# Kernel optimization log

Measured on AMD Instinct MI355X. Metric: run time of the kernel, lower is better.

## Reference

```python
import jax, jax.numpy as jnp
import numpy as np

NUM_CLASSES = 80
IOU_EPS = 1e-5


def _corners(b):
    # NormalizeBoxes with default shape=ones((2,)) divides by 1 -> plain corner transform
    cx, cy, w, h = b[..., 0], b[..., 1], b[..., 2], b[..., 3]
    return cy - h / 2, cx - w / 2, cy + h / 2, cx + w / 2  # y1, x1, y2, x2


def _pairwise_iou(gt, pr):
    # gt: [B,G,4], pr: [P,4] -> [B,G,P]
    ga = gt[..., 2] * gt[..., 3]                      # [B,G]
    pa = pr[:, 2] * pr[:, 3]                          # [P]
    gy1, gx1, gy2, gx2 = _corners(gt)                 # [B,G]
    py1, px1, py2, px2 = _corners(pr)                 # [P]
    ih = jnp.maximum(0.0, jnp.minimum(gy2[..., None], py2) - jnp.maximum(gy1[..., None], py1))
    iw = jnp.maximum(0.0, jnp.minimum(gx2[..., None], px2) - jnp.maximum(gx1[..., None], px1))
    inter = iw * ih
    union = ga[..., None] + pa - inter
    return inter / (union + IOU_EPS)


def _assign_boxes(gt_boxes, pr_boxes):
    B, G, _ = gt_boxes.shape
    P = pr_boxes.shape[1]
    gt_labels = gt_boxes[..., -2]                     # [B,G]
    gt_conf = gt_boxes[..., -1]                       # [B,G]
    pr = pr_boxes[0].astype(jnp.float32)              # priors shared across batch: [P,4]

    iou = _pairwise_iou(gt_boxes[..., :4].astype(jnp.float32), pr)  # [B,G,P]
    valid = (gt_boxes[..., 0] != -1.0).astype(iou.dtype)
    iou = iou * valid[..., None]

    # matches: all pairs with iou>=0.5, plus the argmax prior per valid (conf>0) GT.
    thresh = iou >= 0.5                                             # [B,G,P]
    best_p = jnp.argmax(iou, axis=-1)                               # [B,G]
    best = (jnp.arange(P)[None, None, :] == best_p[..., None]) & (gt_conf > 0.0)[..., None]

    # thresh matches then best matches -> best overrides thresh; within each
    g_ids = jnp.arange(G)[None, :, None]
    g_thresh = jnp.max(jnp.where(thresh, g_ids, -1), axis=1)        # [B,P]
    g_best = jnp.max(jnp.where(best, g_ids, -1), axis=1)            # [B,P]
    win_g = jnp.where(g_best >= 0, g_best, g_thresh)                # [B,P]
    matched = win_g >= 0

    labels = jnp.take_along_axis(gt_labels, jnp.maximum(win_g, 0), axis=1)  # [B,P]
    cls_id = jnp.where(matched, labels.astype(jnp.int32), NUM_CLASSES)
    onehot = jax.nn.one_hot(cls_id, NUM_CLASSES + 1, dtype=jnp.float32)     # [B,P,C+1]
    assign_mask = onehot[..., -1]                                           # 1 = background
    ignore = jnp.any((iou < 0.5) & (iou >= 0.4), axis=1)                    # [B,P]
    assign_mask = jnp.where(ignore, -1.0, assign_mask)

    # loc targets: tf.scatter_nd SUMS duplicate indices, so each (b,p) target is the
    # sum of encodings over all its matches (thresh + best, duplicates counted twice).
    w = thresh.astype(jnp.float32) + best.astype(jnp.float32)       # [B,G,P]
    gb = gt_boxes[..., :4].astype(jnp.float32)
    safe_log = lambda v: jnp.where(v > 0, jnp.log(jnp.maximum(v, 1e-20)), 0.0)
    W = jnp.sum(w, axis=1)                                          # [B,P] match counts
    S_cx = jnp.einsum('bgp,bg->bp', w, gb[..., 0])
    S_cy = jnp.einsum('bgp,bg->bp', w, gb[..., 1])
    S_lw = jnp.einsum('bgp,bg->bp', w, safe_log(gb[..., 2]))
    S_lh = jnp.einsum('bgp,bg->bp', w, safe_log(gb[..., 3]))
    p_cx, p_cy, p_w, p_h = pr[:, 0], pr[:, 1], pr[:, 2], pr[:, 3]   # [P]
    hat_cx = (S_cx - W * p_cx) / p_w
    hat_cy = (S_cy - W * p_cy) / p_h
    hat_w = S_lw - W * jnp.log(p_w)
    hat_h = S_lh - W * jnp.log(p_h)
    loc_true = jnp.stack([hat_cx, hat_cy, hat_w, hat_h], axis=2)    # [B,P,4]

    cls_true = onehot[..., :NUM_CLASSES]
    return cls_true, loc_true, assign_mask[..., None]


def setup_inputs() -> dict:
    key = jax.random.key(0)
    ks = jax.random.split(key, 8)
    B, G, P = 8, 64, 32768
    NUM_VALID = 48
    g_cx = jax.random.uniform(ks[0], (B, G), minval=0.05, maxval=0.95)
    g_cy = jax.random.uniform(ks[1], (B, G), minval=0.05, maxval=0.95)
    g_w = jax.random.uniform(ks[2], (B, G), minval=0.02, maxval=0.30)
    g_h = jax.random.uniform(ks[3], (B, G), minval=0.02, maxval=0.30)
    labels = jax.random.randint(ks[4], (B, G), 0, NUM_CLASSES).astype(jnp.float32)
    conf = jnp.ones((B, G), dtype=jnp.float32)
    gt = jnp.stack([g_cx, g_cy, g_w, g_h, labels, conf], axis=-1)
    valid = (jnp.arange(G) < NUM_VALID)[None, :, None]
    gt_boxes = jnp.where(valid, gt, -1.0)  # pad trailing GTs with -1 (conf -1 <= 0)
    p_cx = jax.random.uniform(ks[5], (P,), minval=0.0, maxval=1.0)
    p_cy = jax.random.uniform(ks[6], (P,), minval=0.0, maxval=1.0)
    pwh = jax.random.uniform(ks[7], (P, 2), minval=0.02, maxval=0.30)
    pr = jnp.concatenate([p_cx[:, None], p_cy[:, None], pwh], axis=1)
    pr_boxes = jnp.broadcast_to(pr[None], (B, P, 4))
    return {"gt_boxes": gt_boxes, "pr_boxes": pr_boxes}


def reference(gt_boxes, pr_boxes):
    return _assign_boxes(gt_boxes, pr_boxes)
```

## Files before the change

### kernel.cpp

```cpp
#include <hip/hip_runtime.h>
#include <cmath>

#define NBATCH 8
#define NGT    64
#define NPR    32768
#define NC     80

__global__ __launch_bounds__(256) void k_bestp(const float* __restrict__ gt,
                                               const float* __restrict__ pr,
                                               int* __restrict__ bestp) {
#pragma clang fp contract(off)
    const int bg  = blockIdx.x;
    const int tid = threadIdx.x;
    const float* g6 = gt + (size_t)bg * 6;
    const float gcx = g6[0], gcy = g6[1], gw = g6[2], gh = g6[3];
    const bool  valid = (gcx != -1.0f);
    const float gy1 = gcy - gh * 0.5f;
    const float gx1 = gcx - gw * 0.5f;
    const float gy2 = gcy + gh * 0.5f;
    const float gx2 = gcx + gw * 0.5f;
    const float ga  = gw * gh;

    float best = -1.0f;
    int   bidx = 0;
    for (int p = tid; p < NPR; p += 256) {
        float4 pv = ((const float4*)pr)[p];
        float py1 = pv.y - pv.w * 0.5f;
        float px1 = pv.x - pv.z * 0.5f;
        float py2 = pv.y + pv.w * 0.5f;
        float px2 = pv.x + pv.z * 0.5f;
        float pa  = pv.z * pv.w;
        float ih  = fmaxf(0.0f, fminf(gy2, py2) - fmaxf(gy1, py1));
        float iw  = fmaxf(0.0f, fminf(gx2, px2) - fmaxf(gx1, px1));
        float inter = iw * ih;
        float uni   = ga + pa - inter;
        float iou   = inter / (uni + 1e-5f);
        iou = valid ? iou : 0.0f;
        if (iou > best) { best = iou; bidx = p; }
    }

    __shared__ float rv[256];
    __shared__ int   ri[256];
    rv[tid] = best; ri[tid] = bidx;
    __syncthreads();
    for (int s = 128; s > 0; s >>= 1) {
        if (tid < s) {
            float v2 = rv[tid + s]; int i2 = ri[tid + s];
            if (v2 > rv[tid] || (v2 == rv[tid] && i2 < ri[tid])) {
                rv[tid] = v2; ri[tid] = i2;
            }
        }
        __syncthreads();
    }
    if (tid == 0) bestp[bg] = ri[0];
}

__global__ __launch_bounds__(256) void k_assign(const float* __restrict__ gt,
                                                const float* __restrict__ pr,
                                                const int* __restrict__ bestp,
                                                float* __restrict__ out_cls,
                                                float* __restrict__ out_loc,
                                                float* __restrict__ out_msk) {
#pragma clang fp contract(off)
    const int b   = blockIdx.y;
    const int tid = threadIdx.x;
    const int p   = blockIdx.x * 256 + tid;

    __shared__ float s_cx[NGT], s_cy[NGT], s_y1[NGT], s_x1[NGT], s_y2[NGT], s_x2[NGT];
    __shared__ float s_ga[NGT], s_lw[NGT], s_lh[NGT], s_lab[NGT], s_conf[NGT];
    __shared__ int   s_bp[NGT], s_val[NGT];
    __shared__ int   s_cls[256];

    if (tid < NGT) {
        const float* g6 = gt + ((size_t)b * NGT + tid) * 6;
        float cx = g6[0], cy = g6[1], w = g6[2], h = g6[3];
        s_cx[tid] = cx; s_cy[tid] = cy;
        s_y1[tid] = cy - h * 0.5f;
        s_x1[tid] = cx - w * 0.5f;
        s_y2[tid] = cy + h * 0.5f;
        s_x2[tid] = cx + w * 0.5f;
        s_ga[tid] = w * h;
        s_lw[tid] = (w > 0.0f) ? logf(fmaxf(w, 1e-20f)) : 0.0f;
        s_lh[tid] = (h > 0.0f) ? logf(fmaxf(h, 1e-20f)) : 0.0f;
        s_lab[tid]  = g6[4];
        s_conf[tid] = g6[5];
        s_val[tid]  = (cx != -1.0f) ? 1 : 0;
        s_bp[tid]   = bestp[b * NGT + tid];
    }
    __syncthreads();

    float4 pv = ((const float4*)pr)[p];
    const float px = pv.x, py = pv.y, pw = pv.z, ph = pv.w;
    const float py1 = py - ph * 0.5f;
    const float px1 = px - pw * 0.5f;
    const float py2 = py + ph * 0.5f;
    const float px2 = px + pw * 0.5f;
    const float pa  = pw * ph;

    int  g_th = -1, g_bs = -1;
    bool ignore = false;
    float W = 0.0f, Scx = 0.0f, Scy = 0.0f, Slw = 0.0f, Slh = 0.0f;

    for (int g = 0; g < NGT; ++g) {
        float ih = fmaxf(0.0f, fminf(s_y2[g], py2) - fmaxf(s_y1[g], py1));
        float iw = fmaxf(0.0f, fminf(s_x2[g], px2) - fmaxf(s_x1[g], px1));
        float inter = iw * ih;
        float uni   = s_ga[g] + pa - inter;
        float iou   = inter / (uni + 1e-5f);
        iou = s_val[g] ? iou : 0.0f;
        bool th = (iou >= 0.5f);
        bool bs = (s_bp[g] == p) && (s_conf[g] > 0.0f);
        if (th) g_th = g;
        if (bs) g_bs = g;
        ignore = ignore || (iou < 0.5f && iou >= 0.4f);
        float wg = (float)th + (float)bs;
        W   += wg;
        Scx += wg * s_cx[g];
        Scy += wg * s_cy[g];
        Slw += wg * s_lw[g];
        Slh += wg * s_lh[g];
    }

    const int  win     = (g_bs >= 0) ? g_bs : g_th;
    const bool matched = (win >= 0);
    const int  cls     = matched ? (int)s_lab[win] : NC;
    float msk = matched ? 0.0f : 1.0f;
    if (ignore) msk = -1.0f;

    const float hcx = (Scx - W * px) / pw;
    const float hcy = (Scy - W * py) / ph;
    const float hw  = Slw - W * logf(pw);
    const float hh  = Slh - W * logf(ph);

    const size_t bp_i = (size_t)b * NPR + p;
    ((float4*)out_loc)[bp_i] = make_float4(hcx, hcy, hw, hh);
    out_msk[bp_i] = msk;

    s_cls[tid] = cls;
    __syncthreads();
    const size_t base4 = ((size_t)b * NPR + (size_t)blockIdx.x * 256) * NC / 4;
    float4* oc4 = (float4*)out_cls;
    #pragma unroll
    for (int k = 0; k < (256 * NC / 4) / 256; ++k) {
        int idx = tid + k * 256;
        int e0  = idx * 4;
        int pl  = e0 / NC;
        int c0  = e0 - pl * NC;
        int cl  = s_cls[pl];
        float4 v;
        v.x = (c0     == cl) ? 1.0f : 0.0f;
        v.y = (c0 + 1 == cl) ? 1.0f : 0.0f;
        v.z = (c0 + 2 == cl) ? 1.0f : 0.0f;
        v.w = (c0 + 3 == cl) ? 1.0f : 0.0f;
        oc4[base4 + idx] = v;
    }
}

extern "C" void kernel_launch(void* const* d_in, const int* in_sizes, int n_in,
                              void* d_out, int out_size, void* d_ws, size_t ws_size,
                              hipStream_t stream) {
    const float* gt = (const float*)d_in[0];
    const float* pr = (const float*)d_in[1];
    int* bestp = (int*)d_ws;

    float* out_cls = (float*)d_out;
    float* out_loc = out_cls + (size_t)NBATCH * NPR * NC;
    float* out_msk = out_loc + (size_t)NBATCH * NPR * 4;

    k_bestp<<<NBATCH * NGT, 256, 0, stream>>>(gt, pr, bestp);
    dim3 g2(NPR / 256, NBATCH);
    k_assign<<<g2, 256, 0, stream>>>(gt, pr, bestp, out_cls, out_loc, out_msk);
}
```

Measured before the change: 154.1 us.

## Split best-prior argmax into chunked multi-GT blocks with wave-shuffle reduction

The best-prior search now gives each block 8 ground-truth boxes and one of 16 prior chunks. Each prior load is reused across 8 GTs held in registers, and the reduction uses wavefront shuffles instead of a shared-memory tree. Per-chunk partial results go to workspace, and the assign kernel's prologue merges them. The goal is to cut redundant prior reads and sync-heavy reductions, and to use more blocks in parallel. In exchange it adds register pressure and a small extra merge step.

```diff
diff --git a/kernel.cpp b/kernel.cpp
--- a/kernel.cpp
+++ b/kernel.cpp
@@ -6,58 +6,104 @@
 #define NPR    32768
 #define NC     80
 
-__global__ __launch_bounds__(256) void k_bestp(const float* __restrict__ gt,
-                                               const float* __restrict__ pr,
-                                               int* __restrict__ bestp) {
+#define CHUNKS 16
+#define CHUNK  (NPR / CHUNKS)
+#define GTPB   8
+
+__global__ __launch_bounds__(256) void k_bestp_part(const float* __restrict__ gt,
+                                                    const float* __restrict__ pr,
+                                                    float* __restrict__ pval,
+                                                    int* __restrict__ pidx) {
 #pragma clang fp contract(off)
-    const int bg  = blockIdx.x;
-    const int tid = threadIdx.x;
-    const float* g6 = gt + (size_t)bg * 6;
-    const float gcx = g6[0], gcy = g6[1], gw = g6[2], gh = g6[3];
-    const bool  valid = (gcx != -1.0f);
-    const float gy1 = gcy - gh * 0.5f;
-    const float gx1 = gcx - gw * 0.5f;
-    const float gy2 = gcy + gh * 0.5f;
-    const float gx2 = gcx + gw * 0.5f;
-    const float ga  = gw * gh;
-
-    float best = -1.0f;
-    int   bidx = 0;
-    for (int p = tid; p < NPR; p += 256) {
+    const int chunk = blockIdx.x;
+    const int gg    = blockIdx.y;
+    const int tid   = threadIdx.x;
+
+    __shared__ float sy1[GTPB], sx1[GTPB], sy2[GTPB], sx2[GTPB], sga[GTPB];
+    __shared__ int   sv[GTPB];
+    if (tid < GTPB) {
+        const float* g6 = gt + ((size_t)gg * GTPB + tid) * 6;
+        float cx = g6[0], cy = g6[1], w = g6[2], h = g6[3];
+        sy1[tid] = cy - h * 0.5f;
+        sx1[tid] = cx - w * 0.5f;
+        sy2[tid] = cy + h * 0.5f;
+        sx2[tid] = cx + w * 0.5f;
+        sga[tid] = w * h;
+        sv[tid]  = (cx != -1.0f) ? 1 : 0;
+    }
+    __syncthreads();
+
+    float gy1[GTPB], gx1[GTPB], gy2[GTPB], gx2[GTPB], ga[GTPB];
+    int   gv[GTPB];
+    #pragma unroll
+    for (int j = 0; j < GTPB; ++j) {
+        gy1[j] = sy1[j]; gx1[j] = sx1[j]; gy2[j] = sy2[j]; gx2[j] = sx2[j];
+        ga[j] = sga[j]; gv[j] = sv[j];
+    }
+
+    float best[GTPB]; int bi[GTPB];
+    #pragma unroll
+    for (int j = 0; j < GTPB; ++j) { best[j] = -1.0f; bi[j] = 0; }
+
+    const int base = chunk * CHUNK;
+    #pragma unroll 4
+    for (int k = 0; k < CHUNK / 256; ++k) {
+        int p = base + k * 256 + tid;
         float4 pv = ((const float4*)pr)[p];
         float py1 = pv.y - pv.w * 0.5f;
         float px1 = pv.x - pv.z * 0.5f;
         float py2 = pv.y + pv.w * 0.5f;
         float px2 = pv.x + pv.z * 0.5f;
         float pa  = pv.z * pv.w;
-        float ih  = fmaxf(0.0f, fminf(gy2, py2) - fmaxf(gy1, py1));
-        float iw  = fmaxf(0.0f, fminf(gx2, px2) - fmaxf(gx1, px1));
-        float inter = iw * ih;
-        float uni   = ga + pa - inter;
-        float iou   = inter / (uni + 1e-5f);
-        iou = valid ? iou : 0.0f;
-        if (iou > best) { best = iou; bidx = p; }
-    }
-
-    __shared__ float rv[256];
-    __shared__ int   ri[256];
-    rv[tid] = best; ri[tid] = bidx;
-    __syncthreads();
-    for (int s = 128; s > 0; s >>= 1) {
-        if (tid < s) {
-            float v2 = rv[tid + s]; int i2 = ri[tid + s];
-            if (v2 > rv[tid] || (v2 == rv[tid] && i2 < ri[tid])) {
-                rv[tid] = v2; ri[tid] = i2;
+        #pragma unroll
+        for (int j = 0; j < GTPB; ++j) {
+            float ih = fmaxf(0.0f, fminf(gy2[j], py2) - fmaxf(gy1[j], py1));
+            float iw = fmaxf(0.0f, fminf(gx2[j], px2) - fmaxf(gx1[j], px1));
+            float inter = iw * ih;
+            float uni   = ga[j] + pa - inter;
+            float iou   = inter / (uni + 1e-5f);
+            iou = gv[j] ? iou : 0.0f;
+            if (iou > best[j]) { best[j] = iou; bi[j] = p; }
+        }
+    }
+
+    #pragma unroll
+    for (int j = 0; j < GTPB; ++j) {
+        #pragma unroll
+        for (int off = 32; off > 0; off >>= 1) {
+            float ov = __shfl_down(best[j], off);
+            int   oi = __shfl_down(bi[j], off);
+            if (ov > best[j] || (ov == best[j] && oi < bi[j])) {
+                best[j] = ov; bi[j] = oi;
             }
         }
-        __syncthreads();
-    }
-    if (tid == 0) bestp[bg] = ri[0];
+    }
+
+    __shared__ float rv[4][GTPB];
+    __shared__ int   rix[4][GTPB];
+    const int wave = tid >> 6;
+    if ((tid & 63) == 0) {
+        #pragma unroll
+        for (int j = 0; j < GTPB; ++j) { rv[wave][j] = best[j]; rix[wave][j] = bi[j]; }
+    }
+    __syncthreads();
+    if (tid < GTPB) {
+        float v = rv[0][tid]; int i = rix[0][tid];
+        #pragma unroll
+        for (int w = 1; w < 4; ++w) {
+            float v2 = rv[w][tid]; int i2 = rix[w][tid];
+            if (v2 > v || (v2 == v && i2 < i)) { v = v2; i = i2; }
+        }
+        int bg = gg * GTPB + tid;
+        pval[bg * CHUNKS + chunk] = v;
+        pidx[bg * CHUNKS + chunk] = i;
+    }
 }
 
 __global__ __launch_bounds__(256) void k_assign(const float* __restrict__ gt,
                                                 const float* __restrict__ pr,
-                                                const int* __restrict__ bestp,
+                                                const float* __restrict__ pval,
+                                                const int* __restrict__ pidx,
                                                 float* __restrict__ out_cls,
                                                 float* __restrict__ out_loc,
                                                 float* __restrict__ out_msk) {
@@ -85,7 +131,14 @@
         s_lab[tid]  = g6[4];
         s_conf[tid] = g6[5];
         s_val[tid]  = (cx != -1.0f) ? 1 : 0;
-        s_bp[tid]   = bestp[b * NGT + tid];
+        int bg = b * NGT + tid;
+        float v = pval[bg * CHUNKS + 0]; int i = pidx[bg * CHUNKS + 0];
+        #pragma unroll
+        for (int c = 1; c < CHUNKS; ++c) {
+            float v2 = pval[bg * CHUNKS + c]; int i2 = pidx[bg * CHUNKS + c];
+            if (v2 > v || (v2 == v && i2 < i)) { v = v2; i = i2; }
+        }
+        s_bp[tid] = i;
     }
     __syncthreads();
 
@@ -161,13 +214,17 @@
                               hipStream_t stream) {
     const float* gt = (const float*)d_in[0];
     const float* pr = (const float*)d_in[1];
-    int* bestp = (int*)d_ws;
+
+    float* pval = (float*)d_ws;
+    int*   pidx = (int*)((char*)d_ws + NBATCH * NGT * CHUNKS * sizeof(float));
 
     float* out_cls = (float*)d_out;
     float* out_loc = out_cls + (size_t)NBATCH * NPR * NC;
     float* out_msk = out_loc + (size_t)NBATCH * NPR * 4;
 
-    k_bestp<<<NBATCH * NGT, 256, 0, stream>>>(gt, pr, bestp);
+    dim3 g1(CHUNKS, NBATCH * NGT / GTPB);
+    k_bestp_part<<<g1, 256, 0, stream>>>(gt, pr, pval, pidx);
+
     dim3 g2(NPR / 256, NBATCH);
-    k_assign<<<g2, 256, 0, stream>>>(gt, pr, bestp, out_cls, out_loc, out_msk);
+    k_assign<<<g2, 256, 0, stream>>>(gt, pr, pval, pidx, out_cls, out_loc, out_msk);
 }
```

Result: faster. 134.1 us (-13.0%).
